# Kernel tuning notes

Hardware: AMD Instinct MI355X
Metric: run time of the kernel (lower is better)

## Reference

```python
import jax, jax.numpy as jnp
import numpy as np

MEM_DIM = 2048
BATCH = 4096


def setup_inputs() -> dict:
    key = jax.random.key(0)
    ks = jax.random.split(key, 8)
    D = MEM_DIM
    scale = 1.0 / np.sqrt(D)  # torch nn.Linear default init range ~ U(-1/sqrt(D), 1/sqrt(D))
    lc = jax.random.normal(ks[0], (BATCH, D), dtype=jnp.float32)
    lh = jax.random.normal(ks[1], (BATCH, D), dtype=jnp.float32)
    rc = jax.random.normal(ks[2], (BATCH, D), dtype=jnp.float32)
    rh = jax.random.normal(ks[3], (BATCH, D), dtype=jnp.float32)
    # Fused params: columns [0:D]=input gate, [D:2D]=left forget, [2D:3D]=right forget, [3D:4D]=update
    Wl = jax.random.uniform(ks[4], (D, 4 * D), dtype=jnp.float32, minval=-scale, maxval=scale)
    Wr = jax.random.uniform(ks[5], (D, 4 * D), dtype=jnp.float32, minval=-scale, maxval=scale)
    bl = jax.random.uniform(ks[6], (4 * D,), dtype=jnp.float32, minval=-scale, maxval=scale)
    br = jax.random.uniform(ks[7], (4 * D,), dtype=jnp.float32, minval=-scale, maxval=scale)
    return {"lc": lc, "lh": lh, "rc": rc, "rh": rh, "Wl": Wl, "bl": bl, "Wr": Wr, "br": br}


def reference(lc, lh, rc, rh, Wl, bl, Wr, br):
    D = lh.shape[-1]
    # Two fused GEMMs replace 8 separate mem_dim x mem_dim linears (same math).
    g = jnp.dot(lh, Wl) + bl + jnp.dot(rh, Wr) + br  # [B, 4D]
    i = jax.nn.sigmoid(g[:, 0 * D:1 * D])   # input gate
    lf = jax.nn.sigmoid(g[:, 1 * D:2 * D])  # left forget gate
    rf = jax.nn.sigmoid(g[:, 2 * D:3 * D])  # right forget gate
    u = jnp.tanh(g[:, 3 * D:4 * D])         # cell update
    c = i * u + lf * lc + rf * rc
    h = jnp.tanh(c)
    return (c, h)
```

## Files before the change

### kernel.cpp

```cpp
#include <hip/hip_runtime.h>
#include <stdint.h>

#define D_MEM 2048
#define BATCH 4096
#define K_DIM 4096
#define N_DIM 8192

typedef __bf16 bf16x8 __attribute__((ext_vector_type(8)));
typedef float f32x4 __attribute__((ext_vector_type(4)));

typedef const void __attribute__((address_space(1)))* gas_t;
typedef void __attribute__((address_space(3)))* las_t;

__device__ __forceinline__ ushort f2b(float f) {
  union { float f; uint32_t u; } v; v.f = f;
  uint32_t u = v.u + 0x7fffu + ((v.u >> 16) & 1u);
  return (ushort)(u >> 16);
}
__device__ __forceinline__ float sigm(float x) {
  return 1.0f / (1.0f + __expf(-x));
}
__device__ __forceinline__ float fast_tanh(float x) {
  float xx = fminf(fmaxf(x, -15.f), 15.f);
  float t = __expf(-2.f * xx);
  return (1.f - t) / (1.f + t);
}

__global__ void cast_concat_kernel(const float* __restrict__ lh,
                                   const float* __restrict__ rh,
                                   ushort* __restrict__ A) {
  int i4 = blockIdx.x * 256 + threadIdx.x;
  int row = i4 >> 10;
  int col = (i4 & 1023) * 4;
  const float* src = (col < D_MEM) ? (lh + (size_t)row * D_MEM + col)
                                   : (rh + (size_t)row * D_MEM + (col - D_MEM));
  float4 v = *(const float4*)src;
  ushort4 o; o.x = f2b(v.x); o.y = f2b(v.y); o.z = f2b(v.z); o.w = f2b(v.w);
  *(ushort4*)(A + (size_t)row * K_DIM + col) = o;
}

__global__ void transpose_cast_kernel(const float* __restrict__ Wl,
                                      const float* __restrict__ Wr,
                                      ushort* __restrict__ Bt) {
  __shared__ float t[64 * 65];
  const float* W = blockIdx.z ? Wr : Wl;
  int n0 = blockIdx.x * 64;
  int k0 = blockIdx.y * 64;
  int tid = threadIdx.x;
#pragma unroll
  for (int i = 0; i < 4; ++i) {
    int idx = i * 256 + tid;
    int rr = idx >> 4;
    int c4 = (idx & 15) * 4;
    float4 v = *(const float4*)(W + (size_t)(k0 + rr) * N_DIM + n0 + c4);
    t[rr * 65 + c4 + 0] = v.x;
    t[rr * 65 + c4 + 1] = v.y;
    t[rr * 65 + c4 + 2] = v.z;
    t[rr * 65 + c4 + 3] = v.w;
  }
  __syncthreads();
  int kbase = (blockIdx.z ? D_MEM : 0) + k0;
  int g  = n0 >> 11;
  int jb = n0 & 2047;
#pragma unroll
  for (int i = 0; i < 4; ++i) {
    int idx = i * 256 + tid;
    int rr = idx >> 4;
    int c4 = (idx & 15) * 4;
    int j = jb + rr;
    int np = ((j >> 5) << 7) + (((j >> 4) & 1) << 6) + (g << 4) + (j & 15);
    ushort4 o;
    o.x = f2b(t[(c4 + 0) * 65 + rr]);
    o.y = f2b(t[(c4 + 1) * 65 + rr]);
    o.z = f2b(t[(c4 + 2) * 65 + rr]);
    o.w = f2b(t[(c4 + 3) * 65 + rr]);
    *(ushort4*)(Bt + (size_t)np * K_DIM + kbase + c4) = o;
  }
}

__global__ __launch_bounds__(256) void gemm_gate_kernel(
    const ushort* __restrict__ A,
    const ushort* __restrict__ B,
    const float* __restrict__ bl,
    const float* __restrict__ br,
    const float* __restrict__ lc,
    const float* __restrict__ rc,
    float* __restrict__ out) {
  const int K = K_DIM;
  __shared__ ushort As[128 * 64];
  __shared__ ushort Bs[128 * 64];
  int tid = threadIdx.x;
  int lane = tid & 63;
  int wave = tid >> 6;
  int wm = wave >> 1, wn = wave & 1;
  int q = lane >> 4, r = lane & 15;
  int m0 = blockIdx.y * 128, n0 = blockIdx.x * 128;

  int c_chunk = (tid & 7) ^ ((tid >> 3) & 7);
  int srow = tid >> 3;
  const ushort* pA = A + (size_t)(m0 + srow) * K + c_chunk * 8;
  const ushort* pB = B + (size_t)(n0 + srow) * K + c_chunk * 8;

  int aoff[4], boff[4];
#pragma unroll
  for (int f = 0; f < 4; ++f) {
    int ml = wm * 64 + f * 16 + r;
    aoff[f] = (ml * 8 + (q ^ (ml & 7))) * 16;
    int nl = wn * 64 + f * 16 + r;
    boff[f] = (nl * 8 + (q ^ (nl & 7))) * 16;
  }

  f32x4 acc[4][4];
#pragma unroll
  for (int i = 0; i < 4; ++i)
#pragma unroll
    for (int j = 0; j < 4; ++j) acc[i][j] = f32x4{0.f, 0.f, 0.f, 0.f};

  char* AsB = (char*)As;
  char* BsB = (char*)Bs;
  int ldsbase = wave * 1024;

  for (int kt = 0; kt < K / 64; ++kt) {
#pragma unroll
    for (int t2 = 0; t2 < 4; ++t2)
      __builtin_amdgcn_global_load_lds((gas_t)(pA + (size_t)t2 * 32 * K),
                                       (las_t)(AsB + t2 * 4096 + ldsbase),
                                       16, 0, 0);
#pragma unroll
    for (int t2 = 0; t2 < 4; ++t2)
      __builtin_amdgcn_global_load_lds((gas_t)(pB + (size_t)t2 * 32 * K),
                                       (las_t)(BsB + t2 * 4096 + ldsbase),
                                       16, 0, 0);
    __syncthreads();
#pragma unroll
    for (int ks = 0; ks < 2; ++ks) {
      bf16x8 af[4], bg[4];
#pragma unroll
      for (int f = 0; f < 4; ++f) {
        af[f] = *(const bf16x8*)(AsB + (aoff[f] ^ (ks * 64)));
        bg[f] = *(const bf16x8*)(BsB + (boff[f] ^ (ks * 64)));
      }
#pragma unroll
      for (int i = 0; i < 4; ++i)
#pragma unroll
        for (int j = 0; j < 4; ++j)
          acc[i][j] = __builtin_amdgcn_mfma_f32_16x16x32_bf16(
              af[i], bg[j], acc[i][j], 0, 0, 0);
    }
    __syncthreads();
    pA += 64;
    pB += 64;
  }

  int colb = (blockIdx.x << 5) + (wn << 4) + r;
  float bsum0 = bl[0 * D_MEM + colb] + br[0 * D_MEM + colb];
  float bsum1 = bl[1 * D_MEM + colb] + br[1 * D_MEM + colb];
  float bsum2 = bl[2 * D_MEM + colb] + br[2 * D_MEM + colb];
  float bsum3 = bl[3 * D_MEM + colb] + br[3 * D_MEM + colb];
  float* outc = out;
  float* outh = out + (size_t)BATCH * D_MEM;
#pragma unroll
  for (int i = 0; i < 4; ++i) {
    int mb = m0 + wm * 64 + i * 16 + q * 4;
#pragma unroll
    for (int e = 0; e < 4; ++e) {
      size_t off = (size_t)(mb + e) * D_MEM + colb;
      float gi = acc[i][0][e] + bsum0;
      float gf = acc[i][1][e] + bsum1;
      float gr = acc[i][2][e] + bsum2;
      float gu = acc[i][3][e] + bsum3;
      float cc = sigm(gi) * fast_tanh(gu) + sigm(gf) * lc[off] + sigm(gr) * rc[off];
      outc[off] = cc;
      outh[off] = fast_tanh(cc);
    }
  }
}

extern "C" void kernel_launch(void* const* d_in, const int* in_sizes, int n_in,
                              void* d_out, int out_size, void* d_ws, size_t ws_size,
                              hipStream_t stream) {
  const float* lc = (const float*)d_in[0];
  const float* lh = (const float*)d_in[1];
  const float* rc = (const float*)d_in[2];
  const float* rh = (const float*)d_in[3];
  const float* Wl = (const float*)d_in[4];
  const float* bl = (const float*)d_in[5];
  const float* Wr = (const float*)d_in[6];
  const float* br = (const float*)d_in[7];
  float* out = (float*)d_out;

  char* ws = (char*)d_ws;
  ushort* A  = (ushort*)ws;
  ushort* Bt = (ushort*)(ws + (size_t)32 * 1024 * 1024);

  cast_concat_kernel<<<16384, 256, 0, stream>>>(lh, rh, A);
  dim3 tg(128, 32, 2);
  transpose_cast_kernel<<<tg, 256, 0, stream>>>(Wl, Wr, Bt);
  dim3 gg(64, 32);
  gemm_gate_kernel<<<gg, 256, 0, stream>>>(A, Bt, bl, br, lc, rc, out);
}
```

Measured before the change: 600.4 us.

## Stage gate epilogue through LDS for coalesced float4 loads and stores

```diff
diff --git a/kernel.cpp b/kernel.cpp
--- a/kernel.cpp
+++ b/kernel.cpp
@@ -18,25 +18,28 @@
   return (ushort)(u >> 16);
 }
 __device__ __forceinline__ float sigm(float x) {
-  return 1.0f / (1.0f + __expf(-x));
+  return __builtin_amdgcn_rcpf(1.0f + __expf(-x));
 }
 __device__ __forceinline__ float fast_tanh(float x) {
   float xx = fminf(fmaxf(x, -15.f), 15.f);
   float t = __expf(-2.f * xx);
-  return (1.f - t) / (1.f + t);
+  return (1.f - t) * __builtin_amdgcn_rcpf(1.f + t);
 }
 
 __global__ void cast_concat_kernel(const float* __restrict__ lh,
                                    const float* __restrict__ rh,
                                    ushort* __restrict__ A) {
-  int i4 = blockIdx.x * 256 + threadIdx.x;
-  int row = i4 >> 10;
-  int col = (i4 & 1023) * 4;
-  const float* src = (col < D_MEM) ? (lh + (size_t)row * D_MEM + col)
-                                   : (rh + (size_t)row * D_MEM + (col - D_MEM));
-  float4 v = *(const float4*)src;
-  ushort4 o; o.x = f2b(v.x); o.y = f2b(v.y); o.z = f2b(v.z); o.w = f2b(v.w);
-  *(ushort4*)(A + (size_t)row * K_DIM + col) = o;
+#pragma unroll
+  for (int it = 0; it < 8; ++it) {
+    int i4 = blockIdx.x * 2048 + it * 256 + threadIdx.x;
+    int row = i4 >> 10;
+    int col = (i4 & 1023) * 4;
+    const float* src = (col < D_MEM) ? (lh + (size_t)row * D_MEM + col)
+                                     : (rh + (size_t)row * D_MEM + (col - D_MEM));
+    float4 v = *(const float4*)src;
+    ushort4 o; o.x = f2b(v.x); o.y = f2b(v.y); o.z = f2b(v.z); o.w = f2b(v.w);
+    *(ushort4*)(A + (size_t)row * K_DIM + col) = o;
+  }
 }
 
 __global__ void transpose_cast_kernel(const float* __restrict__ Wl,
@@ -78,6 +81,10 @@
   }
 }
 
+__device__ __forceinline__ int sw(int row, int col) {
+  return row * 32 + ((((col >> 2) ^ (row & 7)) << 2) | (col & 3));
+}
+
 __global__ __launch_bounds__(256) void gemm_gate_kernel(
     const ushort* __restrict__ A,
     const ushort* __restrict__ B,
@@ -87,8 +94,8 @@
     const float* __restrict__ rc,
     float* __restrict__ out) {
   const int K = K_DIM;
-  __shared__ ushort As[128 * 64];
-  __shared__ ushort Bs[128 * 64];
+  __shared__ __align__(16) char smem[32768];
+  float* smemF = (float*)smem;
   int tid = threadIdx.x;
   int lane = tid & 63;
   int wave = tid >> 6;
@@ -116,8 +123,8 @@
 #pragma unroll
     for (int j = 0; j < 4; ++j) acc[i][j] = f32x4{0.f, 0.f, 0.f, 0.f};
 
-  char* AsB = (char*)As;
-  char* BsB = (char*)Bs;
+  char* AsB = smem;
+  char* BsB = smem + 16384;
   int ldsbase = wave * 1024;
 
   for (int kt = 0; kt < K / 64; ++kt) {
@@ -152,27 +159,55 @@
     pB += 64;
   }
 
-  int colb = (blockIdx.x << 5) + (wn << 4) + r;
+  float* S = smemF;
+  float* T = smemF + 4096;
+  int c0 = blockIdx.x * 32;
+#pragma unroll
+  for (int it = 0; it < 4; ++it) {
+    int idx = it * 256 + tid;
+    int rrow = idx >> 3;
+    int cc4 = (idx & 7) * 4;
+    int slot = sw(rrow, cc4);
+    size_t goff = (size_t)(m0 + rrow) * D_MEM + c0 + cc4;
+    *(float4*)(S + slot) = *(const float4*)(lc + goff);
+    *(float4*)(T + slot) = *(const float4*)(rc + goff);
+  }
+  __syncthreads();
+
+  int colL = wn * 16 + r;
+  int colb = c0 + colL;
   float bsum0 = bl[0 * D_MEM + colb] + br[0 * D_MEM + colb];
   float bsum1 = bl[1 * D_MEM + colb] + br[1 * D_MEM + colb];
   float bsum2 = bl[2 * D_MEM + colb] + br[2 * D_MEM + colb];
   float bsum3 = bl[3 * D_MEM + colb] + br[3 * D_MEM + colb];
-  float* outc = out;
-  float* outh = out + (size_t)BATCH * D_MEM;
 #pragma unroll
   for (int i = 0; i < 4; ++i) {
-    int mb = m0 + wm * 64 + i * 16 + q * 4;
+    int rbase = wm * 64 + i * 16 + q * 4;
 #pragma unroll
     for (int e = 0; e < 4; ++e) {
-      size_t off = (size_t)(mb + e) * D_MEM + colb;
+      int slot = sw(rbase + e, colL);
       float gi = acc[i][0][e] + bsum0;
       float gf = acc[i][1][e] + bsum1;
       float gr = acc[i][2][e] + bsum2;
       float gu = acc[i][3][e] + bsum3;
-      float cc = sigm(gi) * fast_tanh(gu) + sigm(gf) * lc[off] + sigm(gr) * rc[off];
-      outc[off] = cc;
-      outh[off] = fast_tanh(cc);
+      float cc = sigm(gi) * fast_tanh(gu) + sigm(gf) * S[slot] + sigm(gr) * T[slot];
+      S[slot] = cc;
+      T[slot] = fast_tanh(cc);
     }
+  }
+  __syncthreads();
+
+  float* outc = out;
+  float* outh = out + (size_t)BATCH * D_MEM;
+#pragma unroll
+  for (int it = 0; it < 4; ++it) {
+    int idx = it * 256 + tid;
+    int rrow = idx >> 3;
+    int cc4 = (idx & 7) * 4;
+    int slot = sw(rrow, cc4);
+    size_t goff = (size_t)(m0 + rrow) * D_MEM + c0 + cc4;
+    *(float4*)(outc + goff) = *(float4*)(S + slot);
+    *(float4*)(outh + goff) = *(float4*)(T + slot);
   }
 }
 
@@ -193,7 +228,7 @@
   ushort* A  = (ushort*)ws;
   ushort* Bt = (ushort*)(ws + (size_t)32 * 1024 * 1024);
 
-  cast_concat_kernel<<<16384, 256, 0, stream>>>(lh, rh, A);
+  cast_concat_kernel<<<2048, 256, 0, stream>>>(lh, rh, A);
   dim3 tg(128, 32, 2);
   transpose_cast_kernel<<<tg, 256, 0, stream>>>(Wl, Wr, Bt);
   dim3 gg(64, 32);
```

Result: faster. 555.7 us (-7.4%).
